# Optimization experiments

Hardware: AMD Instinct MI355X
Metric: run time of the kernel (lower is better)

The kernel has to match this reference:

```python
import jax, jax.numpy as jnp
import numpy as np


def setup_inputs() -> dict:
    key = jax.random.key(0)
    B, N, M, D = 8, 256, 16, 256
    embeddings = jax.random.normal(key, (B, N, M, D), dtype=jnp.float32)
    w = jnp.asarray(10.0, dtype=jnp.float32)
    b = jnp.asarray(-5.0, dtype=jnp.float32)
    return {"embeddings": embeddings, "w": w, "b": b}


def reference(embeddings, w, b):
    # embeddings: [B, N, M, D]
    B, N, M, D = embeddings.shape
    centroids = jnp.mean(embeddings, axis=2)  # [B, N, D]

    # Cross similarities: S[b,j,i,k] = w * <e_{bji}, c_{bk}> + b
    S = w * jnp.einsum('bjid,bkd->bjik', embeddings, centroids) + b  # [B,N,M,N]

    # Own-centroid case (j == k): leave-one-out centroid
    # <e, (M*c_j - e)/(M-1)> = (M*<e,c_j> - ||e||^2) / (M-1)
    dot_own = jnp.einsum('bjid,bjd->bji', embeddings, centroids)     # [B,N,M]
    sq_norm = jnp.sum(embeddings * embeddings, axis=-1)              # [B,N,M]
    S_self = w * (M * dot_own - sq_norm) / (M - 1) + b               # [B,N,M]

    # Place S_self on the k == j diagonal
    eye = jnp.eye(N, dtype=bool)[None, :, None, :]                   # [1,N,1,N]
    S = jnp.where(eye, S_self[..., None], S)

    # loss = sum log sum_k exp(S) - sum_{j==k} S
    loss = jnp.sum(jax.nn.logsumexp(S, axis=-1)) - jnp.sum(S_self)
    return loss
```

## Files before the change

kernel.cpp:

```cpp
#include <hip/hip_runtime.h>

constexpr int B = 8, N = 256, M = 16, D = 256;

typedef short bf16x8 __attribute__((ext_vector_type(8)));
typedef float f32x4 __attribute__((ext_vector_type(4)));

__device__ __forceinline__ unsigned short f2bf(float x) {
  unsigned u = __float_as_uint(x);
  u = (u + 0x7FFFu + ((u >> 16) & 1u)) >> 16;
  return (unsigned short)u;
}
__device__ __forceinline__ uint4 packbf8(const float* f) {
  uint4 u;
  u.x = (unsigned)f2bf(f[0]) | ((unsigned)f2bf(f[1]) << 16);
  u.y = (unsigned)f2bf(f[2]) | ((unsigned)f2bf(f[3]) << 16);
  u.z = (unsigned)f2bf(f[4]) | ((unsigned)f2bf(f[5]) << 16);
  u.w = (unsigned)f2bf(f[6]) | ((unsigned)f2bf(f[7]) << 16);
  return u;
}


__global__ __launch_bounds__(256) void k_prep(const float* __restrict__ e,
                                              uint4* __restrict__ EbfA,
                                              uint4* __restrict__ Cbf,
                                              float* __restrict__ SQ,
                                              float* __restrict__ out) {
  const int blk = blockIdx.x;
  const int b = blk >> 8, j = blk & 255;
  const int t = threadIdx.x;
  const float* base = e + (size_t)blk * (M * D);

  __shared__ float cbuf[D];
  __shared__ float sqred[4][16];

  float cs = 0.f;
#pragma unroll
  for (int i = 0; i < M; ++i) cs += base[i * D + t];
  cbuf[t] = cs * (1.f / 16.f);

  const int m = t & 15, o2 = t >> 4;
  const float* p0 = base + m * D + o2 * 8;
  float f0[8], f1[8];
  *(float4*)(f0) = *(const float4*)(p0);
  *(float4*)(f0 + 4) = *(const float4*)(p0 + 4);
  *(float4*)(f1) = *(const float4*)(p0 + 128);
  *(float4*)(f1 + 4) = *(const float4*)(p0 + 132);

  EbfA[(size_t)(blk * 8 + (o2 >> 2)) * 64 + (o2 & 3) * 16 + m] = packbf8(f0);
  EbfA[(size_t)(blk * 8 + 4 + (o2 >> 2)) * 64 + (o2 & 3) * 16 + m] = packbf8(f1);

  float sqp = 0.f;
#pragma unroll
  for (int x = 0; x < 8; ++x) sqp = fmaf(f0[x], f0[x], fmaf(f1[x], f1[x], sqp));
  sqp += __shfl_xor(sqp, 16, 64);
  sqp += __shfl_xor(sqp, 32, 64);
  const int w = t >> 6;
  if ((t & 63) < 16) sqred[w][m] = sqp;
  __syncthreads();

  if (t < 32) {
    float cf[8];
#pragma unroll
    for (int x = 0; x < 8; ++x) cf[x] = cbuf[t * 8 + x];
    Cbf[((size_t)(b * 8 + (t >> 2)) * 16 + (j >> 4)) * 64 + (t & 3) * 16 + (j & 15)] =
        packbf8(cf);
  }
  if (t < 16) SQ[blk * 16 + t] = sqred[0][t] + sqred[1][t] + sqred[2][t] + sqred[3][t];
  if (blk == 0 && t == 0) out[0] = 0.f;
}

__global__ __launch_bounds__(256) void k_gemm(const uint4* __restrict__ EbfA,
                                              const uint4* __restrict__ Cbf,
                                              const float* __restrict__ SQ,
                                              const float* __restrict__ wp,
                                              const float* __restrict__ bp,
                                              float* __restrict__ out) {
  const int blk = blockIdx.x;
  const int b = blk >> 6, strip = blk & 63;
  const int tid = threadIdx.x;
  const int wid = tid >> 6, lane = tid & 63;
  const int h = wid >> 1, c = wid & 1;
  const int q = lane >> 4, cl_ = lane & 15;

  const uint4* Ab = EbfA + (size_t)((b * 256 + strip * 4 + h * 2) * 8) * 64 + lane;
  const uint4* Bb = Cbf + (size_t)(b * 128 + c * 8) * 64 + lane;

  f32x4 acc[2][8];
#pragma unroll
  for (int rt = 0; rt < 2; ++rt)
#pragma unroll
    for (int nt = 0; nt < 8; ++nt) acc[rt][nt] = (f32x4)0.f;

#pragma unroll 1
  for (int kc = 0; kc < 8; ++kc) {
    uint4 af0 = Ab[kc * 64];
    uint4 af1 = Ab[(8 + kc) * 64];
    uint4 bfr[8];
#pragma unroll
    for (int nt = 0; nt < 8; ++nt) bfr[nt] = Bb[(kc * 16 + nt) * 64];
    bf16x8 a0 = __builtin_bit_cast(bf16x8, af0);
    bf16x8 a1 = __builtin_bit_cast(bf16x8, af1);
#pragma unroll
    for (int nt = 0; nt < 8; ++nt) {
      bf16x8 bv = __builtin_bit_cast(bf16x8, bfr[nt]);
      acc[0][nt] = __builtin_amdgcn_mfma_f32_16x16x32_bf16(a0, bv, acc[0][nt], 0, 0, 0);
      acc[1][nt] = __builtin_amdgcn_mfma_f32_16x16x32_bf16(a1, bv, acc[1][nt], 0, 0, 0);
    }
  }

  const float w = *wp, bias = *bp;
  __shared__ float lmx[2][64];
  __shared__ float lsm[2][64];
  __shared__ float bred[4];
  float ssum = 0.f;

#pragma unroll
  for (int rt = 0; rt < 2; ++rt) {
    const int jr = strip * 4 + h * 2 + rt;
    const bool own = (c == (jr >> 7)) && (cl_ == (jr & 15));
    const int ntd = (jr >> 4) & 7;
    float sq[4];
    if (own) {
#pragma unroll
      for (int reg = 0; reg < 4; ++reg)
        sq[reg] = SQ[b * 4096 + strip * 64 + (h * 2 + rt) * 16 + q * 4 + reg];
    }
#pragma unroll
    for (int nt = 0; nt < 8; ++nt)
#pragma unroll
      for (int reg = 0; reg < 4; ++reg) {
        const float raw = acc[rt][nt][reg];
        float sv = fmaf(w, raw, bias);
        if (own && nt == ntd) {
          sv = fmaf(w * (1.f / 15.f), 16.f * raw - sq[reg], bias);
          ssum += sv;
        }
        acc[rt][nt][reg] = sv;
      }
#pragma unroll
    for (int reg = 0; reg < 4; ++reg) {
      float mx = acc[rt][0][reg];
#pragma unroll
      for (int nt = 1; nt < 8; ++nt) mx = fmaxf(mx, acc[rt][nt][reg]);
#pragma unroll
      for (int mk = 1; mk < 16; mk <<= 1) mx = fmaxf(mx, __shfl_xor(mx, mk, 64));
      if (cl_ == 0) lmx[c][(h * 2 + rt) * 16 + q * 4 + reg] = mx;
    }
  }
  __syncthreads();

#pragma unroll
  for (int rt = 0; rt < 2; ++rt)
#pragma unroll
    for (int reg = 0; reg < 4; ++reg) {
      const int Rl = (h * 2 + rt) * 16 + q * 4 + reg;
      const float mx = fmaxf(lmx[0][Rl], lmx[1][Rl]);
      float se = 0.f;
#pragma unroll
      for (int nt = 0; nt < 8; ++nt) se += __expf(acc[rt][nt][reg] - mx);
#pragma unroll
      for (int mk = 1; mk < 16; mk <<= 1) se += __shfl_xor(se, mk, 64);
      if (cl_ == 0) lsm[c][Rl] = se;
    }
  __syncthreads();

  float part = -ssum;
  if (c == 0 && cl_ == 0) {
#pragma unroll
    for (int rt = 0; rt < 2; ++rt)
#pragma unroll
      for (int reg = 0; reg < 4; ++reg) {
        const int Rl = (h * 2 + rt) * 16 + q * 4 + reg;
        const float mx = fmaxf(lmx[0][Rl], lmx[1][Rl]);
        part += mx + __logf(lsm[0][Rl] + lsm[1][Rl]);
      }
  }
#pragma unroll
  for (int mk = 1; mk < 64; mk <<= 1) part += __shfl_xor(part, mk, 64);
  if (lane == 0) bred[wid] = part;
  __syncthreads();
  if (tid == 0) atomicAdd(out, bred[0] + bred[1] + bred[2] + bred[3]);
}

extern "C" void kernel_launch(void* const* d_in, const int* in_sizes, int n_in,
                              void* d_out, int out_size, void* d_ws, size_t ws_size,
                              hipStream_t stream) {
  const float* e = (const float*)d_in[0];
  const float* wp = (const float*)d_in[1];
  const float* bp = (const float*)d_in[2];
  float* out = (float*)d_out;
  char* ws = (char*)d_ws;
  uint4* EbfA = (uint4*)ws;
  uint4* Cbf = (uint4*)(ws + (size_t)16 * 1024 * 1024);
  float* SQ = (float*)(ws + (size_t)17 * 1024 * 1024);

  k_prep<<<B * N, 256, 0, stream>>>(e, EbfA, Cbf, SQ, out);
  k_gemm<<<B * 64, 256, 0, stream>>>(EbfA, Cbf, SQ, wp, bp, out);
}
```

Measured before the change: 97.36 us.

## Fuse prep and GEMM into one cooperative kernel with grid sync

Merges the prep and GEMM kernels into a single cooperative kernel. Each block computes centroids and bf16 A-tiles for its own four rows and keeps the A fragments and squared norms in LDS, which avoids writing them to global memory and reading them back. Only the centroids go to global memory, and a grid-wide sync precedes the MFMA GEMM. The aim is to remove one kernel launch and the round trip of the embedding tile through global memory. The cost is a grid barrier and reliance on all 512 blocks being co-resident, with the old two-kernel path kept as a fallback if the cooperative launch fails.

```diff
diff --git a/kernel.cpp b/kernel.cpp
--- a/kernel.cpp
+++ b/kernel.cpp
@@ -1,4 +1,7 @@
 #include <hip/hip_runtime.h>
+#include <hip/hip_cooperative_groups.h>
+
+namespace cg = cooperative_groups;
 
 constexpr int B = 8, N = 256, M = 16, D = 256;
 
@@ -19,6 +22,164 @@
   return u;
 }
 
+__global__ __launch_bounds__(256, 2) void k_fused(const float* __restrict__ e,
+                                                  uint4* __restrict__ Cbf,
+                                                  const float* __restrict__ wp,
+                                                  const float* __restrict__ bp,
+                                                  float* __restrict__ out) {
+  const int blk = blockIdx.x;
+  const int b = blk >> 6, strip = blk & 63;
+  const int tid = threadIdx.x;
+  const int wid = tid >> 6, lane = tid & 63;
+
+  __shared__ uint4 A_lds[4 * 8 * 64];
+  __shared__ float cbuf[4][D];
+  __shared__ float sql[64];
+  __shared__ float lmx[2][64];
+  __shared__ float lsm[2][64];
+  __shared__ float bred[4];
+
+  {
+    const int j = strip * 4 + wid;
+    const float* base = e + (size_t)(b * 256 + j) * (M * D);
+
+    float4 cv = {0.f, 0.f, 0.f, 0.f};
+#pragma unroll
+    for (int i = 0; i < M; ++i) {
+      float4 v = *(const float4*)(base + i * D + lane * 4);
+      cv.x += v.x; cv.y += v.y; cv.z += v.z; cv.w += v.w;
+    }
+    cv.x *= (1.f / 16.f); cv.y *= (1.f / 16.f);
+    cv.z *= (1.f / 16.f); cv.w *= (1.f / 16.f);
+    *(float4*)&cbuf[wid][lane * 4] = cv;
+
+    const int m = lane & 15, q = lane >> 4;
+    const float* rp = base + m * D + q * 8;
+    float sqp = 0.f;
+#pragma unroll
+    for (int kc = 0; kc < 8; ++kc) {
+      float f[8];
+      *(float4*)(f) = *(const float4*)(rp + kc * 32);
+      *(float4*)(f + 4) = *(const float4*)(rp + kc * 32 + 4);
+      A_lds[(wid * 8 + kc) * 64 + lane] = packbf8(f);
+#pragma unroll
+      for (int x = 0; x < 8; ++x) sqp = fmaf(f[x], f[x], sqp);
+    }
+    sqp += __shfl_xor(sqp, 16, 64);
+    sqp += __shfl_xor(sqp, 32, 64);
+    if (q == 0) sql[wid * 16 + m] = sqp;
+  }
+  __syncthreads();
+
+  if (lane < 32) {
+    const int j = strip * 4 + wid;
+    float cf[8];
+#pragma unroll
+    for (int x = 0; x < 8; ++x) cf[x] = cbuf[wid][lane * 8 + x];
+    Cbf[((size_t)(b * 8 + (lane >> 2)) * 16 + (j >> 4)) * 64 + (lane & 3) * 16 +
+        (j & 15)] = packbf8(cf);
+  }
+  if (blk == 0 && tid == 0) out[0] = 0.f;
+
+  cg::this_grid().sync();
+
+  const int h = wid >> 1, c = wid & 1;
+  const int q = lane >> 4, cl_ = lane & 15;
+  const uint4* Bb = Cbf + (size_t)(b * 128 + c * 8) * 64 + lane;
+
+  f32x4 acc[2][8];
+#pragma unroll
+  for (int rt = 0; rt < 2; ++rt)
+#pragma unroll
+    for (int nt = 0; nt < 8; ++nt) acc[rt][nt] = (f32x4)0.f;
+
+#pragma unroll 1
+  for (int kc = 0; kc < 8; ++kc) {
+    uint4 af0 = A_lds[((h * 2) * 8 + kc) * 64 + lane];
+    uint4 af1 = A_lds[((h * 2 + 1) * 8 + kc) * 64 + lane];
+    uint4 bfr[8];
+#pragma unroll
+    for (int nt = 0; nt < 8; ++nt) bfr[nt] = Bb[(kc * 16 + nt) * 64];
+    bf16x8 a0 = __builtin_bit_cast(bf16x8, af0);
+    bf16x8 a1 = __builtin_bit_cast(bf16x8, af1);
+#pragma unroll
+    for (int nt = 0; nt < 8; ++nt) {
+      bf16x8 bv = __builtin_bit_cast(bf16x8, bfr[nt]);
+      acc[0][nt] = __builtin_amdgcn_mfma_f32_16x16x32_bf16(a0, bv, acc[0][nt], 0, 0, 0);
+      acc[1][nt] = __builtin_amdgcn_mfma_f32_16x16x32_bf16(a1, bv, acc[1][nt], 0, 0, 0);
+    }
+  }
+
+  const float w = *wp, bias = *bp;
+  float ssum = 0.f;
+
+#pragma unroll
+  for (int rt = 0; rt < 2; ++rt) {
+    const int jr = strip * 4 + h * 2 + rt;
+    const bool own = (c == (jr >> 7)) && (cl_ == (jr & 15));
+    const int ntd = (jr >> 4) & 7;
+    float sq[4];
+    if (own) {
+#pragma unroll
+      for (int reg = 0; reg < 4; ++reg)
+        sq[reg] = sql[(h * 2 + rt) * 16 + q * 4 + reg];
+    }
+#pragma unroll
+    for (int nt = 0; nt < 8; ++nt)
+#pragma unroll
+      for (int reg = 0; reg < 4; ++reg) {
+        const float raw = acc[rt][nt][reg];
+        float sv = fmaf(w, raw, bias);
+        if (own && nt == ntd) {
+          sv = fmaf(w * (1.f / 15.f), 16.f * raw - sq[reg], bias);
+          ssum += sv;
+        }
+        acc[rt][nt][reg] = sv;
+      }
+#pragma unroll
+    for (int reg = 0; reg < 4; ++reg) {
+      float mx = acc[rt][0][reg];
+#pragma unroll
+      for (int nt = 1; nt < 8; ++nt) mx = fmaxf(mx, acc[rt][nt][reg]);
+#pragma unroll
+      for (int mk = 1; mk < 16; mk <<= 1) mx = fmaxf(mx, __shfl_xor(mx, mk, 64));
+      if (cl_ == 0) lmx[c][(h * 2 + rt) * 16 + q * 4 + reg] = mx;
+    }
+  }
+  __syncthreads();
+
+#pragma unroll
+  for (int rt = 0; rt < 2; ++rt)
+#pragma unroll
+    for (int reg = 0; reg < 4; ++reg) {
+      const int Rl = (h * 2 + rt) * 16 + q * 4 + reg;
+      const float mx = fmaxf(lmx[0][Rl], lmx[1][Rl]);
+      float se = 0.f;
+#pragma unroll
+      for (int nt = 0; nt < 8; ++nt) se += __expf(acc[rt][nt][reg] - mx);
+#pragma unroll
+      for (int mk = 1; mk < 16; mk <<= 1) se += __shfl_xor(se, mk, 64);
+      if (cl_ == 0) lsm[c][Rl] = se;
+    }
+  __syncthreads();
+
+  float part = -ssum;
+  if (c == 0 && cl_ == 0) {
+#pragma unroll
+    for (int rt = 0; rt < 2; ++rt)
+#pragma unroll
+      for (int reg = 0; reg < 4; ++reg) {
+        const int Rl = (h * 2 + rt) * 16 + q * 4 + reg;
+        const float mx = fmaxf(lmx[0][Rl], lmx[1][Rl]);
+        part += mx + __logf(lsm[0][Rl] + lsm[1][Rl]);
+      }
+  }
+#pragma unroll
+  for (int mk = 1; mk < 64; mk <<= 1) part += __shfl_xor(part, mk, 64);
+  if (lane == 0) bred[wid] = part;
+  __syncthreads();
+  if (tid == 0) atomicAdd(out, bred[0] + bred[1] + bred[2] + bred[3]);
+}
 
 __global__ __launch_bounds__(256) void k_prep(const float* __restrict__ e,
                                               uint4* __restrict__ EbfA,
@@ -194,6 +355,11 @@
   uint4* Cbf = (uint4*)(ws + (size_t)16 * 1024 * 1024);
   float* SQ = (float*)(ws + (size_t)17 * 1024 * 1024);
 
-  k_prep<<<B * N, 256, 0, stream>>>(e, EbfA, Cbf, SQ, out);
-  k_gemm<<<B * 64, 256, 0, stream>>>(EbfA, Cbf, SQ, wp, bp, out);
-}
+  void* args[] = {(void*)&e, (void*)&Cbf, (void*)&wp, (void*)&bp, (void*)&out};
+  hipError_t err = hipLaunchCooperativeKernel((const void*)k_fused, dim3(B * 64),
+                                              dim3(256), args, 0, stream);
+  if (err != hipSuccess) {
+    k_prep<<<B * N, 256, 0, stream>>>(e, EbfA, Cbf, SQ, out);
+    k_gemm<<<B * 64, 256, 0, stream>>>(EbfA, Cbf, SQ, wp, bp, out);
+  }
+}
```

Result: slower. 162.9 us (+67.3%).

## Fuse bf16 conversion and squared norms into GEMM kernel via LDS staging

Applied to the files above, without the earlier changes.

The prep kernel now only computes centroids. The GEMM kernel loads its own fp32 embedding rows, converts them to bf16 into shared memory, and computes the squared norms locally. This removes the global write and re-read of the bf16 embedding copy and the SQ array. The cost is a second fp32 read of the embeddings, since the centroid kernel also reads them, and the GEMM kernel has to convert before it starts computing.

```diff
diff --git a/kernel.cpp b/kernel.cpp
--- a/kernel.cpp
+++ b/kernel.cpp
@@ -20,10 +20,8 @@
 }
 
 
-__global__ __launch_bounds__(256) void k_prep(const float* __restrict__ e,
-                                              uint4* __restrict__ EbfA,
+__global__ __launch_bounds__(256) void k_cent(const float* __restrict__ e,
                                               uint4* __restrict__ Cbf,
-                                              float* __restrict__ SQ,
                                               float* __restrict__ out) {
   const int blk = blockIdx.x;
   const int b = blk >> 8, j = blk & 255;
@@ -31,31 +29,10 @@
   const float* base = e + (size_t)blk * (M * D);
 
   __shared__ float cbuf[D];
-  __shared__ float sqred[4][16];
-
   float cs = 0.f;
 #pragma unroll
   for (int i = 0; i < M; ++i) cs += base[i * D + t];
   cbuf[t] = cs * (1.f / 16.f);
-
-  const int m = t & 15, o2 = t >> 4;
-  const float* p0 = base + m * D + o2 * 8;
-  float f0[8], f1[8];
-  *(float4*)(f0) = *(const float4*)(p0);
-  *(float4*)(f0 + 4) = *(const float4*)(p0 + 4);
-  *(float4*)(f1) = *(const float4*)(p0 + 128);
-  *(float4*)(f1 + 4) = *(const float4*)(p0 + 132);
-
-  EbfA[(size_t)(blk * 8 + (o2 >> 2)) * 64 + (o2 & 3) * 16 + m] = packbf8(f0);
-  EbfA[(size_t)(blk * 8 + 4 + (o2 >> 2)) * 64 + (o2 & 3) * 16 + m] = packbf8(f1);
-
-  float sqp = 0.f;
-#pragma unroll
-  for (int x = 0; x < 8; ++x) sqp = fmaf(f0[x], f0[x], fmaf(f1[x], f1[x], sqp));
-  sqp += __shfl_xor(sqp, 16, 64);
-  sqp += __shfl_xor(sqp, 32, 64);
-  const int w = t >> 6;
-  if ((t & 63) < 16) sqred[w][m] = sqp;
   __syncthreads();
 
   if (t < 32) {
@@ -65,24 +42,48 @@
     Cbf[((size_t)(b * 8 + (t >> 2)) * 16 + (j >> 4)) * 64 + (t & 3) * 16 + (j & 15)] =
         packbf8(cf);
   }
-  if (t < 16) SQ[blk * 16 + t] = sqred[0][t] + sqred[1][t] + sqred[2][t] + sqred[3][t];
   if (blk == 0 && t == 0) out[0] = 0.f;
 }
 
-__global__ __launch_bounds__(256) void k_gemm(const uint4* __restrict__ EbfA,
-                                              const uint4* __restrict__ Cbf,
-                                              const float* __restrict__ SQ,
-                                              const float* __restrict__ wp,
-                                              const float* __restrict__ bp,
-                                              float* __restrict__ out) {
+__global__ __launch_bounds__(256) void k_gemm2(const float* __restrict__ e,
+                                               const uint4* __restrict__ Cbf,
+                                               const float* __restrict__ wp,
+                                               const float* __restrict__ bp,
+                                               float* __restrict__ out) {
   const int blk = blockIdx.x;
   const int b = blk >> 6, strip = blk & 63;
   const int tid = threadIdx.x;
   const int wid = tid >> 6, lane = tid & 63;
+
+  __shared__ uint4 A_lds[4 * 8 * 64];
+  __shared__ float sql[64];
+  __shared__ float lmx[2][64];
+  __shared__ float lsm[2][64];
+  __shared__ float bred[4];
+
+  {
+    const int j = strip * 4 + wid;
+    const float* base = e + (size_t)(b * 256 + j) * (M * D);
+    const int m = lane & 15, q = lane >> 4;
+    const float* rp = base + m * D + q * 8;
+    float sqp = 0.f;
+#pragma unroll
+    for (int kc = 0; kc < 8; ++kc) {
+      float f[8];
+      *(float4*)(f) = *(const float4*)(rp + kc * 32);
+      *(float4*)(f + 4) = *(const float4*)(rp + kc * 32 + 4);
+      A_lds[(wid * 8 + kc) * 64 + lane] = packbf8(f);
+#pragma unroll
+      for (int x = 0; x < 8; ++x) sqp = fmaf(f[x], f[x], sqp);
+    }
+    sqp += __shfl_xor(sqp, 16, 64);
+    sqp += __shfl_xor(sqp, 32, 64);
+    if (q == 0) sql[wid * 16 + m] = sqp;
+  }
+  __syncthreads();
+
   const int h = wid >> 1, c = wid & 1;
   const int q = lane >> 4, cl_ = lane & 15;
-
-  const uint4* Ab = EbfA + (size_t)((b * 256 + strip * 4 + h * 2) * 8) * 64 + lane;
   const uint4* Bb = Cbf + (size_t)(b * 128 + c * 8) * 64 + lane;
 
   f32x4 acc[2][8];
@@ -93,8 +94,8 @@
 
 #pragma unroll 1
   for (int kc = 0; kc < 8; ++kc) {
-    uint4 af0 = Ab[kc * 64];
-    uint4 af1 = Ab[(8 + kc) * 64];
+    uint4 af0 = A_lds[((h * 2) * 8 + kc) * 64 + lane];
+    uint4 af1 = A_lds[((h * 2 + 1) * 8 + kc) * 64 + lane];
     uint4 bfr[8];
 #pragma unroll
     for (int nt = 0; nt < 8; ++nt) bfr[nt] = Bb[(kc * 16 + nt) * 64];
@@ -109,9 +110,6 @@
   }
 
   const float w = *wp, bias = *bp;
-  __shared__ float lmx[2][64];
-  __shared__ float lsm[2][64];
-  __shared__ float bred[4];
   float ssum = 0.f;
 
 #pragma unroll
@@ -123,7 +121,7 @@
     if (own) {
 #pragma unroll
       for (int reg = 0; reg < 4; ++reg)
-        sq[reg] = SQ[b * 4096 + strip * 64 + (h * 2 + rt) * 16 + q * 4 + reg];
+        sq[reg] = sql[(h * 2 + rt) * 16 + q * 4 + reg];
     }
 #pragma unroll
     for (int nt = 0; nt < 8; ++nt)
@@ -189,11 +187,8 @@
   const float* wp = (const float*)d_in[1];
   const float* bp = (const float*)d_in[2];
   float* out = (float*)d_out;
-  char* ws = (char*)d_ws;
-  uint4* EbfA = (uint4*)ws;
-  uint4* Cbf = (uint4*)(ws + (size_t)16 * 1024 * 1024);
-  float* SQ = (float*)(ws + (size_t)17 * 1024 * 1024);
+  uint4* Cbf = (uint4*)d_ws;
 
-  k_prep<<<B * N, 256, 0, stream>>>(e, EbfA, Cbf, SQ, out);
-  k_gemm<<<B * 64, 256, 0, stream>>>(EbfA, Cbf, SQ, wp, bp, out);
+  k_cent<<<B * N, 256, 0, stream>>>(e, Cbf, out);
+  k_gemm2<<<B * 64, 256, 0, stream>>>(e, Cbf, wp, bp, out);
 }
```

After: 99.58 us. +2.3%, slower.
